# Kernel tuning notes

Hardware: AMD Instinct MI355X
Metric: run time of the kernel (lower is better)

## Reference

```python
import jax, jax.numpy as jnp
import numpy as np

B, N = 8192, 64
EPS = 1e-3  # diagonal jitter to guarantee SPD


def setup_inputs() -> dict:
    key = jax.random.key(0)
    A = jax.random.normal(key, (B, N, N), dtype=jnp.float32)
    # SPD: X = A A^T / N + eps*I  (eigenvalues strictly positive)
    X = jnp.einsum('bij,bkj->bik', A, A) / N + EPS * jnp.eye(N, dtype=jnp.float32)
    return {"X": X}


def reference(X) -> jnp.ndarray:
    # torch.linalg.eigh -> jnp.linalg.eigh (batched symmetric eigendecomposition)
    eigvals, eigvecs = jnp.linalg.eigh(X)            # [B,N], [B,N,N]
    log_eigvals = jnp.log(eigvals)                   # [B,N]
    # eigvecs @ diag(log_eigvals) @ eigvecs^T, fused as scaled-column GEMM
    return jnp.einsum('bik,bk,bjk->bij', eigvecs, log_eigvals, eigvecs)
```

## Files before the change

### kernel.cpp

```cpp
#include <hip/hip_runtime.h>
#include <cmath>


#define MAXSWEEP 16
#define JTOL 2e-4f
#define XTOL 2e-3f
#define TSTRIDE 68

typedef float f32x2 __attribute__((ext_vector_type(2)));

__global__ __launch_bounds__(64, 2)
void logeig_kernel(const float* __restrict__ X, float* __restrict__ Out, int B)
{
    const int lane = threadIdx.x & 63;
    const long b = blockIdx.x;

    __shared__ float T[64 * TSTRIDE];

    const float* Xb = X + b * 4096;
    float*       Ob = Out + b * 4096;
    float4*      myrow = reinterpret_cast<float4*>(T + lane * TSTRIDE);

    f32x2 fv[32];
#pragma unroll
    for (int i = 0; i < 16; ++i) {
        const float4 v = reinterpret_cast<const float4*>(Xb + lane * 64)[i];
        fv[2*i+0] = f32x2{v.x, v.y};
        fv[2*i+1] = f32x2{v.z, v.w};
        myrow[i] = v;
    }
    __builtin_amdgcn_wave_barrier();

    float app;
    {
        f32x2 a0 = {0.f,0.f}, a1 = {0.f,0.f}, a2 = {0.f,0.f}, a3 = {0.f,0.f};
#pragma unroll
        for (int i = 0; i < 32; i += 4) {
            a0 = __builtin_elementwise_fma(fv[i+0], fv[i+0], a0);
            a1 = __builtin_elementwise_fma(fv[i+1], fv[i+1], a1);
            a2 = __builtin_elementwise_fma(fv[i+2], fv[i+2], a2);
            a3 = __builtin_elementwise_fma(fv[i+3], fv[i+3], a3);
        }
        const f32x2 at = (a0 + a1) + (a2 + a3);
        app = at.x + at.y;
    }
    float rho = 1.0f;

    int quiet = 0;
    for (int sweep = 0; sweep < MAXSWEEP; ++sweep) {
        for (int r = 1; r < 64; ++r) {
            const int partner = lane ^ r;
            const int pa = partner << 2;

            const float aqq  = __int_as_float(
                __builtin_amdgcn_ds_bpermute(pa, __float_as_int(app)));
            const float rhoq = __int_as_float(
                __builtin_amdgcn_ds_bpermute(pa, __float_as_int(rho)));

            const float4* pc = reinterpret_cast<const float4*>(T + partner * TSTRIDE);
            f32x2 tv[32];
#pragma unroll
            for (int i = 0; i < 16; ++i) {
                const float4 v = pc[i];
                tv[2*i+0] = f32x2{v.x, v.y};
                tv[2*i+1] = f32x2{v.z, v.w};
            }
#pragma unroll
            for (int i = 0; i < 32; ++i)
                asm volatile("" : "+v"(tv[i]));

            float apq;
            {
                f32x2 a0 = {0.f,0.f}, a1 = {0.f,0.f}, a2 = {0.f,0.f}, a3 = {0.f,0.f};
#pragma unroll
                for (int i = 0; i < 32; i += 4) {
                    a0 = __builtin_elementwise_fma(fv[i+0], tv[i+0], a0);
                    a1 = __builtin_elementwise_fma(fv[i+1], tv[i+1], a1);
                    a2 = __builtin_elementwise_fma(fv[i+2], tv[i+2], a2);
                    a3 = __builtin_elementwise_fma(fv[i+3], tv[i+3], a3);
                }
                const f32x2 at = (a0 + a1) + (a2 + a3);
                apq = at.x + at.y;
            }

            const float rel = sqrtf(app * aqq);
            const bool rot  = fabsf(apq) > JTOL * rel;
            const bool bigr = __any(fabsf(apq) > XTOL * rel);

            if (__any(rot)) {
                const bool  isp  = lane < partner;
                const float tapp = (rho  * rho ) * app;
                const float taqq = (rhoq * rhoq) * aqq;
                const float prod = (rho * rhoq) * apq;
                const float App = isp ? tapp : taqq;
                const float Aqq = isp ? taqq : tapp;
                const float tau = (Aqq - App) / (2.f * prod);
                const float t0  = copysignf(1.f, tau) / (fabsf(tau) + sqrtf(fmaf(tau, tau, 1.f)));
                const float c0  = rsqrtf(fmaf(t0, t0, 1.f));
                const float tl  = isp ? t0 : -t0;
                const float alpha = rot ? tl * (rhoq * __builtin_amdgcn_rcpf(rho)) : 0.f;

                const f32x2 na2 = {-alpha, -alpha};
#pragma unroll
                for (int i = 0; i < 32; ++i)
                    fv[i] = __builtin_elementwise_fma(na2, tv[i], fv[i]);

                app = rot ? (app - alpha * apq) * fmaf(t0, t0, 1.f) : app;
                rho = rot ? rho * c0 : rho;

                const bool renorm = rot && (app > 1e24f);
                if (__any(renorm)) {
                    const float sc = renorm ? rsqrtf(app) : 1.0f;
                    if (renorm) { rho = rho * (app * sc); app = 1.0f; }
                    const f32x2 sc2 = {sc, sc};
#pragma unroll
                    for (int i = 0; i < 32; ++i) fv[i] = fv[i] * sc2;
                }

                if (rot) {
#pragma unroll
                    for (int i = 0; i < 16; ++i)
                        myrow[i] = float4{fv[2*i+0].x, fv[2*i+0].y,
                                          fv[2*i+1].x, fv[2*i+1].y};
                }
            }
            __builtin_amdgcn_wave_barrier();

            quiet = bigr ? 0 : quiet + 1;
            if (quiet >= 63) break;
        }
        if (quiet >= 63) break;
    }

    float nrm2;
    {
        f32x2 a0 = {0.f,0.f}, a1 = {0.f,0.f}, a2 = {0.f,0.f}, a3 = {0.f,0.f};
#pragma unroll
        for (int i = 0; i < 32; i += 4) {
            a0 = __builtin_elementwise_fma(fv[i+0], fv[i+0], a0);
            a1 = __builtin_elementwise_fma(fv[i+1], fv[i+1], a1);
            a2 = __builtin_elementwise_fma(fv[i+2], fv[i+2], a2);
            a3 = __builtin_elementwise_fma(fv[i+3], fv[i+3], a3);
        }
        const f32x2 at = (a0 + a1) + (a2 + a3);
        nrm2 = at.x + at.y;
    }
    const float wk  = 0.5f * logf((rho * rho) * nrm2);
    const float inv = rsqrtf(nrm2);

#pragma unroll
    for (int i = 0; i < 16; ++i)
        myrow[i] = float4{fv[2*i+0].x * inv, fv[2*i+0].y * inv,
                          fv[2*i+1].x * inv, fv[2*i+1].y * inv};
    T[lane * TSTRIDE + 64] = wk;
    __syncthreads();

    const int la = lane >> 3, lb = lane & 7;
    float acc[8][8];
#pragma unroll
    for (int r0 = 0; r0 < 8; ++r0)
#pragma unroll
        for (int c0 = 0; c0 < 8; ++c0) acc[r0][c0] = 0.f;

#pragma unroll 4
    for (int k = 0; k < 64; ++k) {
        const float wkk = T[k * TSTRIDE + 64];
        const float* row = T + k * TSTRIDE;
        const float4 p0 = *reinterpret_cast<const float4*>(row + la * 8);
        const float4 p1 = *reinterpret_cast<const float4*>(row + la * 8 + 4);
        const float4 u0 = *reinterpret_cast<const float4*>(row + lb * 8);
        const float4 u1 = *reinterpret_cast<const float4*>(row + lb * 8 + 4);
        const float pr[8] = { p0.x*wkk, p0.y*wkk, p0.z*wkk, p0.w*wkk,
                              p1.x*wkk, p1.y*wkk, p1.z*wkk, p1.w*wkk };
        const float uc[8] = { u0.x, u0.y, u0.z, u0.w, u1.x, u1.y, u1.z, u1.w };
#pragma unroll
        for (int r0 = 0; r0 < 8; ++r0)
#pragma unroll
            for (int c0 = 0; c0 < 8; ++c0)
                acc[r0][c0] = fmaf(pr[r0], uc[c0], acc[r0][c0]);
    }

#pragma unroll
    for (int r0 = 0; r0 < 8; ++r0) {
        float* dst = Ob + (la * 8 + r0) * 64 + lb * 8;
        float4 o0 = { acc[r0][0], acc[r0][1], acc[r0][2], acc[r0][3] };
        float4 o1 = { acc[r0][4], acc[r0][5], acc[r0][6], acc[r0][7] };
        reinterpret_cast<float4*>(dst)[0] = o0;
        reinterpret_cast<float4*>(dst)[1] = o1;
    }
}

extern "C" void kernel_launch(void* const* d_in, const int* in_sizes, int n_in,
                              void* d_out, int out_size, void* d_ws, size_t ws_size,
                              hipStream_t stream)
{
    const float* Xp = (const float*)d_in[0];
    float* Op = (float*)d_out;
    const int B = in_sizes[0] / 4096;
    logeig_kernel<<<B, 64, 0, stream>>>(Xp, Op, B);
}
```

Measured before the change: 3.045 ms.

## Use inline-asm LDS b128 accesses, loosen rotation tolerance, defer rho exchange

```diff
diff --git a/kernel.cpp b/kernel.cpp
--- a/kernel.cpp
+++ b/kernel.cpp
@@ -3,11 +3,20 @@
 
 
 #define MAXSWEEP 16
-#define JTOL 2e-4f
+#define JTOL 5e-4f
 #define XTOL 2e-3f
 #define TSTRIDE 68
 
-typedef float f32x2 __attribute__((ext_vector_type(2)));
+typedef float f32x4 __attribute__((ext_vector_type(4)));
+
+#define DS_READ(dst, addr, OFF) \
+    asm volatile("ds_read_b128 %0, %1 offset:" OFF : "=v"(dst) : "v"(addr))
+#define DS_WRITE(addr, src, OFF) \
+    asm volatile("ds_write_b128 %0, %1 offset:" OFF : : "v"(addr), "v"(src) : "memory")
+
+#define FOR16(OP) OP(0,"0") OP(1,"16") OP(2,"32") OP(3,"48") OP(4,"64") OP(5,"80") \
+    OP(6,"96") OP(7,"112") OP(8,"128") OP(9,"144") OP(10,"160") OP(11,"176") \
+    OP(12,"192") OP(13,"208") OP(14,"224") OP(15,"240")
 
 __global__ __launch_bounds__(64, 2)
 void logeig_kernel(const float* __restrict__ X, float* __restrict__ Out, int B)
@@ -19,75 +28,73 @@
 
     const float* Xb = X + b * 4096;
     float*       Ob = Out + b * 4096;
-    float4*      myrow = reinterpret_cast<float4*>(T + lane * TSTRIDE);
-
-    f32x2 fv[32];
-#pragma unroll
-    for (int i = 0; i < 16; ++i) {
-        const float4 v = reinterpret_cast<const float4*>(Xb + lane * 64)[i];
-        fv[2*i+0] = f32x2{v.x, v.y};
-        fv[2*i+1] = f32x2{v.z, v.w};
-        myrow[i] = v;
-    }
-    __builtin_amdgcn_wave_barrier();
+
+    const unsigned tbase = (unsigned)(size_t)(void*)T;
+    const unsigned maddr = tbase + (unsigned)(lane * (TSTRIDE * 4));
+
+    f32x4 fq[16];
+    {
+        const float4* Xr = reinterpret_cast<const float4*>(Xb + lane * 64);
+#pragma unroll
+        for (int i = 0; i < 16; ++i) {
+            const float4 v = Xr[i];
+            fq[i] = f32x4{v.x, v.y, v.z, v.w};
+        }
+    }
+#define WRF(i, o) DS_WRITE(maddr, fq[i], o);
+    FOR16(WRF)
 
     float app;
     {
-        f32x2 a0 = {0.f,0.f}, a1 = {0.f,0.f}, a2 = {0.f,0.f}, a3 = {0.f,0.f};
-#pragma unroll
-        for (int i = 0; i < 32; i += 4) {
-            a0 = __builtin_elementwise_fma(fv[i+0], fv[i+0], a0);
-            a1 = __builtin_elementwise_fma(fv[i+1], fv[i+1], a1);
-            a2 = __builtin_elementwise_fma(fv[i+2], fv[i+2], a2);
-            a3 = __builtin_elementwise_fma(fv[i+3], fv[i+3], a3);
-        }
-        const f32x2 at = (a0 + a1) + (a2 + a3);
-        app = at.x + at.y;
+        f32x4 a0 = 0.f, a1 = 0.f, a2 = 0.f, a3 = 0.f;
+#pragma unroll
+        for (int i = 0; i < 16; i += 4) {
+            a0 = __builtin_elementwise_fma(fq[i+0], fq[i+0], a0);
+            a1 = __builtin_elementwise_fma(fq[i+1], fq[i+1], a1);
+            a2 = __builtin_elementwise_fma(fq[i+2], fq[i+2], a2);
+            a3 = __builtin_elementwise_fma(fq[i+3], fq[i+3], a3);
+        }
+        const f32x4 s = (a0 + a1) + (a2 + a3);
+        app = (s.x + s.y) + (s.z + s.w);
     }
     float rho = 1.0f;
-
     int quiet = 0;
+
     for (int sweep = 0; sweep < MAXSWEEP; ++sweep) {
         for (int r = 1; r < 64; ++r) {
             const int partner = lane ^ r;
-            const int pa = partner << 2;
-
-            const float aqq  = __int_as_float(
-                __builtin_amdgcn_ds_bpermute(pa, __float_as_int(app)));
-            const float rhoq = __int_as_float(
-                __builtin_amdgcn_ds_bpermute(pa, __float_as_int(rho)));
-
-            const float4* pc = reinterpret_cast<const float4*>(T + partner * TSTRIDE);
-            f32x2 tv[32];
-#pragma unroll
-            for (int i = 0; i < 16; ++i) {
-                const float4 v = pc[i];
-                tv[2*i+0] = f32x2{v.x, v.y};
-                tv[2*i+1] = f32x2{v.z, v.w};
-            }
-#pragma unroll
-            for (int i = 0; i < 32; ++i)
-                asm volatile("" : "+v"(tv[i]));
+            const unsigned paddr = tbase + (unsigned)(partner * (TSTRIDE * 4));
+
+            const float aqq = __int_as_float(
+                __builtin_amdgcn_ds_bpermute(partner << 2, __float_as_int(app)));
+
+            f32x4 tq[16];
+#define RDT(i, o) DS_READ(tq[i], paddr, o);
+            FOR16(RDT)
+            asm volatile("s_waitcnt lgkmcnt(0)" ::: "memory");
+            __builtin_amdgcn_sched_barrier(0);
 
             float apq;
             {
-                f32x2 a0 = {0.f,0.f}, a1 = {0.f,0.f}, a2 = {0.f,0.f}, a3 = {0.f,0.f};
-#pragma unroll
-                for (int i = 0; i < 32; i += 4) {
-                    a0 = __builtin_elementwise_fma(fv[i+0], tv[i+0], a0);
-                    a1 = __builtin_elementwise_fma(fv[i+1], tv[i+1], a1);
-                    a2 = __builtin_elementwise_fma(fv[i+2], tv[i+2], a2);
-                    a3 = __builtin_elementwise_fma(fv[i+3], tv[i+3], a3);
+                f32x4 a0 = 0.f, a1 = 0.f, a2 = 0.f, a3 = 0.f;
+#pragma unroll
+                for (int i = 0; i < 16; i += 4) {
+                    a0 = __builtin_elementwise_fma(fq[i+0], tq[i+0], a0);
+                    a1 = __builtin_elementwise_fma(fq[i+1], tq[i+1], a1);
+                    a2 = __builtin_elementwise_fma(fq[i+2], tq[i+2], a2);
+                    a3 = __builtin_elementwise_fma(fq[i+3], tq[i+3], a3);
                 }
-                const f32x2 at = (a0 + a1) + (a2 + a3);
-                apq = at.x + at.y;
+                const f32x4 s = (a0 + a1) + (a2 + a3);
+                apq = (s.x + s.y) + (s.z + s.w);
             }
 
-            const float rel = sqrtf(app * aqq);
-            const bool rot  = fabsf(apq) > JTOL * rel;
-            const bool bigr = __any(fabsf(apq) > XTOL * rel);
+            const float rel  = sqrtf(app * aqq);
+            const bool  rot  = fabsf(apq) > JTOL * rel;
+            const bool  bigr = __any(fabsf(apq) > XTOL * rel);
 
             if (__any(rot)) {
+                const float rhoq = __int_as_float(
+                    __builtin_amdgcn_ds_bpermute(partner << 2, __float_as_int(rho)));
                 const bool  isp  = lane < partner;
                 const float tapp = (rho  * rho ) * app;
                 const float taqq = (rhoq * rhoq) * aqq;
@@ -100,11 +107,10 @@
                 const float tl  = isp ? t0 : -t0;
                 const float alpha = rot ? tl * (rhoq * __builtin_amdgcn_rcpf(rho)) : 0.f;
 
-                const f32x2 na2 = {-alpha, -alpha};
-#pragma unroll
-                for (int i = 0; i < 32; ++i)
-                    fv[i] = __builtin_elementwise_fma(na2, tv[i], fv[i]);
-
+                const f32x4 na = {-alpha, -alpha, -alpha, -alpha};
+#pragma unroll
+                for (int i = 0; i < 16; ++i)
+                    fq[i] = __builtin_elementwise_fma(na, tq[i], fq[i]);
                 app = rot ? (app - alpha * apq) * fmaf(t0, t0, 1.f) : app;
                 rho = rot ? rho * c0 : rho;
 
@@ -112,16 +118,13 @@
                 if (__any(renorm)) {
                     const float sc = renorm ? rsqrtf(app) : 1.0f;
                     if (renorm) { rho = rho * (app * sc); app = 1.0f; }
-                    const f32x2 sc2 = {sc, sc};
-#pragma unroll
-                    for (int i = 0; i < 32; ++i) fv[i] = fv[i] * sc2;
+                    const f32x4 sc4 = {sc, sc, sc, sc};
+#pragma unroll
+                    for (int i = 0; i < 16; ++i) fq[i] = fq[i] * sc4;
                 }
 
                 if (rot) {
-#pragma unroll
-                    for (int i = 0; i < 16; ++i)
-                        myrow[i] = float4{fv[2*i+0].x, fv[2*i+0].y,
-                                          fv[2*i+1].x, fv[2*i+1].y};
+                    FOR16(WRF)
                 }
             }
             __builtin_amdgcn_wave_barrier();
@@ -134,24 +137,23 @@
 
     float nrm2;
     {
-        f32x2 a0 = {0.f,0.f}, a1 = {0.f,0.f}, a2 = {0.f,0.f}, a3 = {0.f,0.f};
-#pragma unroll
-        for (int i = 0; i < 32; i += 4) {
-            a0 = __builtin_elementwise_fma(fv[i+0], fv[i+0], a0);
-            a1 = __builtin_elementwise_fma(fv[i+1], fv[i+1], a1);
-            a2 = __builtin_elementwise_fma(fv[i+2], fv[i+2], a2);
-            a3 = __builtin_elementwise_fma(fv[i+3], fv[i+3], a3);
-        }
-        const f32x2 at = (a0 + a1) + (a2 + a3);
-        nrm2 = at.x + at.y;
+        f32x4 a0 = 0.f, a1 = 0.f, a2 = 0.f, a3 = 0.f;
+#pragma unroll
+        for (int i = 0; i < 16; i += 4) {
+            a0 = __builtin_elementwise_fma(fq[i+0], fq[i+0], a0);
+            a1 = __builtin_elementwise_fma(fq[i+1], fq[i+1], a1);
+            a2 = __builtin_elementwise_fma(fq[i+2], fq[i+2], a2);
+            a3 = __builtin_elementwise_fma(fq[i+3], fq[i+3], a3);
+        }
+        const f32x4 s = (a0 + a1) + (a2 + a3);
+        nrm2 = (s.x + s.y) + (s.z + s.w);
     }
     const float wk  = 0.5f * logf((rho * rho) * nrm2);
     const float inv = rsqrtf(nrm2);
-
-#pragma unroll
-    for (int i = 0; i < 16; ++i)
-        myrow[i] = float4{fv[2*i+0].x * inv, fv[2*i+0].y * inv,
-                          fv[2*i+1].x * inv, fv[2*i+1].y * inv};
+    const f32x4 inv4 = {inv, inv, inv, inv};
+
+#define WRU(i, o) { const f32x4 u##i = fq[i] * inv4; DS_WRITE(maddr, u##i, o); }
+    FOR16(WRU)
     T[lane * TSTRIDE + 64] = wk;
     __syncthreads();
 
```

Result: slower. 3.209 ms (+5.4%).

## Use DPP lane exchanges for intra-16 Jacobi rounds instead of LDS

Applied to the files above, without the earlier changes.

```diff
diff --git a/kernel.cpp b/kernel.cpp
--- a/kernel.cpp
+++ b/kernel.cpp
@@ -3,11 +3,99 @@
 
 
 #define MAXSWEEP 16
-#define JTOL 2e-4f
+#define JTOL 5e-4f
 #define XTOL 2e-3f
 #define TSTRIDE 68
 
 typedef float f32x2 __attribute__((ext_vector_type(2)));
+
+template<int CTRL>
+__device__ __forceinline__ float dppf(float x) {
+    return __int_as_float(__builtin_amdgcn_update_dpp(
+        __float_as_int(x), __float_as_int(x), CTRL, 0xF, 0xF, false));
+}
+#define DPP_XOR1  dppf<177>
+#define DPP_XOR2  dppf<78>
+#define DPP_XOR3  dppf<27>
+#define DPP_XOR7  dppf<0x141>
+#define DPP_XOR15 dppf<0x140>
+
+template<int R>
+__device__ __forceinline__ float exch_t(float x) {
+    if constexpr (R & 8) x = DPP_XOR15(x);
+    constexpr int L4 = (R & 8) ? (R ^ 15) : R;
+    if constexpr (L4 & 4) x = DPP_XOR7(x);
+    constexpr int Q = (L4 & 4) ? (L4 ^ 7) : L4;
+    if constexpr (Q == 1) x = DPP_XOR1(x);
+    if constexpr (Q == 2) x = DPP_XOR2(x);
+    if constexpr (Q == 3) x = DPP_XOR3(x);
+    return x;
+}
+template<int R>
+__device__ __forceinline__ f32x2 exch2(f32x2 v) {
+    return f32x2{exch_t<R>(v.x), exch_t<R>(v.y)};
+}
+
+template<int R>
+__device__ __forceinline__ bool valu_round(f32x2 (&fv)[32], float &app,
+                                           float &rho, bool &vdirty, int lane)
+{
+    float aqq  = exch_t<R>(app);
+    float rhoq = exch_t<R>(rho);
+
+    f32x2 a0{0.f,0.f}, a1{0.f,0.f}, a2{0.f,0.f}, a3{0.f,0.f};
+#pragma unroll
+    for (int i = 0; i < 32; i += 4) {
+        const f32x2 t0 = exch2<R>(fv[i+0]);
+        const f32x2 t1 = exch2<R>(fv[i+1]);
+        const f32x2 t2 = exch2<R>(fv[i+2]);
+        const f32x2 t3 = exch2<R>(fv[i+3]);
+        a0 = __builtin_elementwise_fma(fv[i+0], t0, a0);
+        a1 = __builtin_elementwise_fma(fv[i+1], t1, a1);
+        a2 = __builtin_elementwise_fma(fv[i+2], t2, a2);
+        a3 = __builtin_elementwise_fma(fv[i+3], t3, a3);
+    }
+    const f32x2 at = (a0 + a1) + (a2 + a3);
+    const float apq = at.x + at.y;
+
+    const float rel  = sqrtf(app * aqq);
+    const bool  rot  = fabsf(apq) > JTOL * rel;
+    const bool  bigr = __any(fabsf(apq) > XTOL * rel);
+
+    if (__any(rot)) {
+        constexpr int HB = (R >= 8) ? 8 : (R >= 4) ? 4 : (R >= 2) ? 2 : 1;
+        const bool  isp  = (lane & HB) == 0;
+        const float tapp = (rho  * rho ) * app;
+        const float taqq = (rhoq * rhoq) * aqq;
+        const float prod = (rho * rhoq) * apq;
+        const float App = isp ? tapp : taqq;
+        const float Aqq = isp ? taqq : tapp;
+        const float tau = (Aqq - App) / (2.f * prod);
+        const float t0s = copysignf(1.f, tau) / (fabsf(tau) + sqrtf(fmaf(tau, tau, 1.f)));
+        const float c0  = rsqrtf(fmaf(t0s, t0s, 1.f));
+        const float tl  = isp ? t0s : -t0s;
+        const float alpha = rot ? tl * (rhoq * __builtin_amdgcn_rcpf(rho)) : 0.f;
+        const f32x2 na = {-alpha, -alpha};
+#pragma unroll
+        for (int i = 0; i < 32; ++i) {
+            const f32x2 t = exch2<R>(fv[i]);
+            fv[i] = __builtin_elementwise_fma(na, t, fv[i]);
+        }
+        app = rot ? (app - alpha * apq) * fmaf(t0s, t0s, 1.f) : app;
+        rho = rot ? rho * c0 : rho;
+
+        const bool renorm = rot && (app > 1e24f);
+        if (__any(renorm)) {
+            const float sc = renorm ? rsqrtf(app) : 1.0f;
+            if (renorm) { rho = rho * (app * sc); app = 1.0f; }
+            const f32x2 sc2 = {sc, sc};
+#pragma unroll
+            for (int i = 0; i < 32; ++i) fv[i] = fv[i] * sc2;
+        }
+        vdirty = vdirty || rot;
+    }
+    return bigr;
+}
 
 __global__ __launch_bounds__(64, 2)
 void logeig_kernel(const float* __restrict__ X, float* __restrict__ Out, int B)
@@ -45,10 +133,11 @@
         app = at.x + at.y;
     }
     float rho = 1.0f;
-
     int quiet = 0;
-    for (int sweep = 0; sweep < MAXSWEEP; ++sweep) {
-        for (int r = 1; r < 64; ++r) {
+    bool done = false;
+
+    for (int sweep = 0; sweep < MAXSWEEP && !done; ++sweep) {
+        for (int r = 16; r < 64; ++r) {
             const int partner = lane ^ r;
             const int pa = partner << 2;
 
@@ -83,9 +172,9 @@
                 apq = at.x + at.y;
             }
 
-            const float rel = sqrtf(app * aqq);
-            const bool rot  = fabsf(apq) > JTOL * rel;
-            const bool bigr = __any(fabsf(apq) > XTOL * rel);
+            const float rel  = sqrtf(app * aqq);
+            const bool  rot  = fabsf(apq) > JTOL * rel;
+            const bool  bigr = __any(fabsf(apq) > XTOL * rel);
 
             if (__any(rot)) {
                 const bool  isp  = lane < partner;
@@ -100,11 +189,10 @@
                 const float tl  = isp ? t0 : -t0;
                 const float alpha = rot ? tl * (rhoq * __builtin_amdgcn_rcpf(rho)) : 0.f;
 
-                const f32x2 na2 = {-alpha, -alpha};
+                const f32x2 na = {-alpha, -alpha};
 #pragma unroll
                 for (int i = 0; i < 32; ++i)
-                    fv[i] = __builtin_elementwise_fma(na2, tv[i], fv[i]);
-
+                    fv[i] = __builtin_elementwise_fma(na, tv[i], fv[i]);
                 app = rot ? (app - alpha * apq) * fmaf(t0, t0, 1.f) : app;
                 rho = rot ? rho * c0 : rho;
 
@@ -127,9 +215,44 @@
             __builtin_amdgcn_wave_barrier();
 
             quiet = bigr ? 0 : quiet + 1;
-            if (quiet >= 63) break;
-        }
-        if (quiet >= 63) break;
+            if (quiet >= 63) { done = true; break; }
+        }
+
+        bool vdirty = false;
+        if (!done) {
+            for (int r = 1; r < 16; ++r) {
+                bool bigr;
+                switch (r) {
+                  case  1: bigr = valu_round< 1>(fv, app, rho, vdirty, lane); break;
+                  case  2: bigr = valu_round< 2>(fv, app, rho, vdirty, lane); break;
+                  case  3: bigr = valu_round< 3>(fv, app, rho, vdirty, lane); break;
+                  case  4: bigr = valu_round< 4>(fv, app, rho, vdirty, lane); break;
+                  case  5: bigr = valu_round< 5>(fv, app, rho, vdirty, lane); break;
+                  case  6: bigr = valu_round< 6>(fv, app, rho, vdirty, lane); break;
+                  case  7: bigr = valu_round< 7>(fv, app, rho, vdirty, lane); break;
+                  case  8: bigr = valu_round< 8>(fv, app, rho, vdirty, lane); break;
+                  case  9: bigr = valu_round< 9>(fv, app, rho, vdirty, lane); break;
+                  case 10: bigr = valu_round<10>(fv, app, rho, vdirty, lane); break;
+                  case 11: bigr = valu_round<11>(fv, app, rho, vdirty, lane); break;
+                  case 12: bigr = valu_round<12>(fv, app, rho, vdirty, lane); break;
+                  case 13: bigr = valu_round<13>(fv, app, rho, vdirty, lane); break;
+                  case 14: bigr = valu_round<14>(fv, app, rho, vdirty, lane); break;
+                  default: bigr = valu_round<15>(fv, app, rho, vdirty, lane); break;
+                }
+                quiet = bigr ? 0 : quiet + 1;
+                if (quiet >= 63) { done = true; break; }
+            }
+        }
+
+        if (__any(vdirty)) {
+            if (vdirty) {
+#pragma unroll
+                for (int i = 0; i < 16; ++i)
+                    myrow[i] = float4{fv[2*i+0].x, fv[2*i+0].y,
+                                      fv[2*i+1].x, fv[2*i+1].y};
+            }
+        }
+        __builtin_amdgcn_wave_barrier();
     }
 
     float nrm2;
```

Result: slower. 3.289 ms (+8.0%).
